# Optimization experiments

Measured on AMD Instinct MI355X. Metric: run time of the kernel, lower is better.

The kernel has to match this reference:

```python
import jax, jax.numpy as jnp
import numpy as np

B, S, D = 16, 4096, 128
LN_EPS = 1e-5
REC_EPS = 1e-8


def setup_inputs() -> dict:
    key = jax.random.key(0)
    k1, k2, k3, k4 = jax.random.split(key, 4)
    return {
        "C": jax.random.normal(k1, (B, S, D), dtype=jnp.float32),
        "V": jax.random.normal(k2, (B, S, D), dtype=jnp.float32),
        "W": jax.random.normal(k3, (B, S, D), dtype=jnp.float32),
        "encoder_context": jax.random.normal(k4, (B, D), dtype=jnp.float32),
        "time_modulation": jnp.full((1, 1, D), 0.5, dtype=jnp.float32),
        "context_modulation": jnp.full((1, D), 0.5, dtype=jnp.float32),
        "ln_weight": jnp.ones((D,), dtype=jnp.float32),
        "ln_bias": jnp.zeros((D,), dtype=jnp.float32),
    }


def reference(C, V, W, encoder_context, time_modulation, context_modulation, ln_weight, ln_bias):
    b_, s_, d_ = C.shape
    tm = time_modulation[0, 0]  # [D]
    # context gate is time-invariant: compute once
    ctx_add = jax.nn.sigmoid(encoder_context * context_modulation) * encoder_context  # [B,D]

    def step(carry, xs):
        a, bst = carry  # a: [B,1], bst: [B,D]
        c_t, v_t, w_t = xs  # each [B,D]
        decay = jax.nn.sigmoid(w_t * tm)  # [B,D]
        ec = jnp.exp(c_t)  # [B,D]
        a = decay.mean(axis=1, keepdims=True) * a + ec.sum(axis=1, keepdims=True)
        bst = decay * bst + ec * v_t + ctx_add
        out_t = bst / (a + REC_EPS)
        return (a, bst), out_t

    a0 = jnp.zeros((b_, 1), dtype=C.dtype)
    b0 = jnp.zeros((b_, d_), dtype=C.dtype)
    xs = (jnp.swapaxes(C, 0, 1), jnp.swapaxes(V, 0, 1), jnp.swapaxes(W, 0, 1))  # [S,B,D]
    _, ys = jax.lax.scan(step, (a0, b0), xs)  # ys: [S,B,D]
    res = jnp.swapaxes(ys, 0, 1)  # [B,S,D]

    mu = jnp.mean(res, axis=-1, keepdims=True)
    var = jnp.var(res, axis=-1, keepdims=True)
    normed = (res - mu) * jax.lax.rsqrt(var + LN_EPS)
    return normed * ln_weight + ln_bias
```

## Files before the change

kernel.cpp:

```cpp
#include <hip/hip_runtime.h>

#define BB   16
#define SS   4096
#define DD   128
#define NCH  512
#define TT   (SS / NCH)
#define WPB  4
#define NTHR 256

#define DTILE 16
#define SUBS  16
#define CPS   (NCH / SUBS)

#define LN_EPS  1e-5f
#define REC_EPS 1e-8f

__device__ __forceinline__ float fast_rcp(float x) { return __builtin_amdgcn_rcpf(x); }
__device__ __forceinline__ float sigm(float x) { return fast_rcp(1.0f + __expf(-x)); }

__device__ __forceinline__ unsigned pack2(float a, float b) {
    unsigned ua = (__float_as_uint(a) + 0x8000u) >> 16;
    unsigned ub = (__float_as_uint(b) + 0x8000u) & 0xFFFF0000u;
    return ub | ua;
}
__device__ __forceinline__ float up_lo(unsigned u) { return __uint_as_float(u << 16); }
__device__ __forceinline__ float up_hi(unsigned u) { return __uint_as_float(u & 0xFFFF0000u); }

template<int CTRL>
__device__ __forceinline__ float dpp_mov0(float x) {
    return __int_as_float(
        __builtin_amdgcn_update_dpp(0, __float_as_int(x), CTRL, 0xF, 0xF, true));
}

__device__ __forceinline__ void wave_red2(float& a, float& b) {
    a += dpp_mov0<0x111>(a); b += dpp_mov0<0x111>(b);
    a += dpp_mov0<0x112>(a); b += dpp_mov0<0x112>(b);
    a += dpp_mov0<0x114>(a); b += dpp_mov0<0x114>(b);
    a += dpp_mov0<0x118>(a); b += dpp_mov0<0x118>(b);
    a += dpp_mov0<0x142>(a); b += dpp_mov0<0x142>(b);
    a += dpp_mov0<0x143>(a); b += dpp_mov0<0x143>(b);
    a = __int_as_float(__builtin_amdgcn_readlane(__float_as_int(a), 63));
    b = __int_as_float(__builtin_amdgcn_readlane(__float_as_int(b), 63));
}

typedef const __attribute__((address_space(1))) unsigned int gas_u32;
typedef __attribute__((address_space(3))) unsigned int las_u32;
__device__ __forceinline__ void gload_lds16(const void* g, void* l) {
    __builtin_amdgcn_global_load_lds((gas_u32*)g, (las_u32*)l, 16, 0, 0);
}

#define VM_WAIT() asm volatile("s_waitcnt vmcnt(0)" ::: "memory")

__global__ __launch_bounds__(NTHR, 3) void pass1_kernel(
    const float* __restrict__ C, const float* __restrict__ V, const float* __restrict__ W,
    const float* __restrict__ enc, const float* __restrict__ tmod, const float* __restrict__ cmod,
    unsigned* __restrict__ DTb,
    float* __restrict__ Pbuf, float* __restrict__ Qbuf,
    float* __restrict__ PaBuf, float* __restrict__ QaBuf,
    float2* __restrict__ MEbuf)
{
    __shared__ float lds[WPB][3][TT * DD];

    const int wv   = threadIdx.x >> 6;
    const int lane = threadIdx.x & 63;
    const int gc   = blockIdx.x * WPB + wv;
    const int b    = gc >> 9;
    const int ch   = gc & (NCH - 1);
    const int d2   = lane << 1;

    const int t0 = ch * TT;
    const size_t chunk = ((size_t)b * SS + t0) * DD;
    const char* Cc = (const char*)(C + chunk);
    const char* Wc = (const char*)(W + chunk);
    const char* Vc = (const char*)(V + chunk);
    uint2* DTp = (uint2*)(DTb + chunk + d2);

#pragma unroll
    for (int i = 0; i < 4; ++i) {
        const size_t bo = (size_t)i * 1024 + (size_t)lane * 16;
        gload_lds16(Cc + bo, &lds[wv][0][i * 256]);
        gload_lds16(Wc + bo, &lds[wv][1][i * 256]);
        gload_lds16(Vc + bo, &lds[wv][2][i * 256]);
    }

    const float2 tm = *(const float2*)(tmod + d2);
    const float2 cm = *(const float2*)(cmod + d2);
    const float2 ec = *(const float2*)(enc + b * DD + d2);

    VM_WAIT();

    float2 ctx;
    ctx.x = sigm(ec.x * cm.x) * ec.x;
    ctx.y = sigm(ec.y * cm.y) * ec.y;

    float2 P = make_float2(1.f, 1.f);
    float2 Q = make_float2(0.f, 0.f);
    float sdp[TT], sep[TT];

#pragma unroll
    for (int t = 0; t < TT; ++t) {
        const float2 cv = *(const float2*)&lds[wv][0][t * DD + d2];
        const float2 wl = *(const float2*)&lds[wv][1][t * DD + d2];
        const float2 vl = *(const float2*)&lds[wv][2][t * DD + d2];

        float2 dec, e2, T2; uint2 u;
        dec.x = sigm(wl.x * tm.x); dec.y = sigm(wl.y * tm.y);
        e2.x = __expf(cv.x); e2.y = __expf(cv.y);
        T2.x = e2.x * vl.x + ctx.x;
        T2.y = e2.y * vl.y + ctx.y;

        u.x = pack2(dec.x, T2.x); u.y = pack2(dec.y, T2.y);
        DTp[t * (DD / 2)] = u;

        const float dqx = up_lo(u.x), dqy = up_lo(u.y);
        const float tqx = up_hi(u.x), tqy = up_hi(u.y);
        Q.x = dqx * Q.x + tqx;
        Q.y = dqy * Q.y + tqy;
        P.x *= dqx; P.y *= dqy;

        sdp[t] = dec.x + dec.y;
        sep[t] = e2.x + e2.y;
    }

#pragma unroll
    for (int t = 0; t < TT; ++t) wave_red2(sdp[t], sep[t]);

    float pa = 1.f, qa = 0.f;
    float mk = 0.f, ek = 0.f;
#pragma unroll
    for (int t = 0; t < TT; ++t) {
        const float mt = sdp[t] * (1.0f / DD);
        pa *= mt;
        qa = mt * qa + sep[t];
        if (lane == t) { mk = mt; ek = sep[t]; }
    }

    *(float2*)(Pbuf + (size_t)gc * DD + d2) = P;
    *(float2*)(Qbuf + (size_t)gc * DD + d2) = Q;
    if (lane < TT) MEbuf[(size_t)b * SS + t0 + lane] = make_float2(mk, ek);
    if (lane == 0) { PaBuf[gc] = pa; QaBuf[gc] = qa; }
}

__global__ __launch_bounds__(256, 2) void pass2_kernel(
    const float* __restrict__ Pbuf, const float* __restrict__ Qbuf,
    const float* __restrict__ PaBuf, const float* __restrict__ QaBuf,
    float* __restrict__ bst0, float* __restrict__ a0)
{
    const int b   = blockIdx.x >> 3;
    const int dt  = blockIdx.x & 7;
    const int tid = threadIdx.x;
    const int dl  = tid & (DTILE - 1);
    const int sub = tid >> 4;
    const int d   = dt * DTILE + dl;

    __shared__ float cP[SUBS][DTILE], cQ[SUBS][DTILE], ent[SUBS][DTILE];
    __shared__ float sPa[256], sQa[256];

    const int ch0 = sub * CPS;
    const size_t base = ((size_t)b * NCH + ch0) * DD + d;
    float Pr[CPS], Qr[CPS];
    float p = 1.f, q = 0.f;
#pragma unroll
    for (int i = 0; i < CPS; ++i) {
        Pr[i] = Pbuf[base + (size_t)i * DD];
        Qr[i] = Qbuf[base + (size_t)i * DD];
        q = Pr[i] * q + Qr[i];
        p = Pr[i] * p;
    }
    cP[sub][dl] = p; cQ[sub][dl] = q;
    __syncthreads();

    if (tid < DTILE) {
        float s = 0.f;
#pragma unroll
        for (int sb = 0; sb < SUBS; ++sb) {
            ent[sb][tid] = s;
            s = cP[sb][tid] * s + cQ[sb][tid];
        }
    }
    __syncthreads();

    float s = ent[sub][dl];
#pragma unroll
    for (int i = 0; i < CPS; ++i) {
        bst0[base + (size_t)i * DD] = s;
        s = Pr[i] * s + Qr[i];
    }

    if (dt == 0) {
        const int cbase = b * NCH;
        const float p0 = PaBuf[cbase + 2 * tid],     q0 = QaBuf[cbase + 2 * tid];
        const float p1 = PaBuf[cbase + 2 * tid + 1], q1 = QaBuf[cbase + 2 * tid + 1];
        float Pc = p1 * p0;
        float Qc = p1 * q0 + q1;
#pragma unroll
        for (int off = 1; off < 256; off <<= 1) {
            sPa[tid] = Pc; sQa[tid] = Qc;
            __syncthreads();
            if (tid >= off) {
                const float pp = sPa[tid - off], qq = sQa[tid - off];
                Qc = Pc * qq + Qc;
                Pc = Pc * pp;
            }
            __syncthreads();
        }
        sQa[tid] = Qc;
        __syncthreads();
        const float E = (tid == 0) ? 0.f : sQa[tid - 1];
        a0[cbase + 2 * tid]     = E;
        a0[cbase + 2 * tid + 1] = p0 * E + q0;
    }
}

__global__ __launch_bounds__(NTHR, 6) void pass3_kernel(
    const unsigned* __restrict__ DTb,
    const float* __restrict__ lnw, const float* __restrict__ lnb,
    const float* __restrict__ bst0, const float* __restrict__ a0,
    const float2* __restrict__ MEbuf,
    float* __restrict__ out)
{
    __shared__ unsigned lds[WPB][TT * DD];

    const int wv   = threadIdx.x >> 6;
    const int lane = threadIdx.x & 63;
    const int gc   = blockIdx.x * WPB + wv;
    const int b    = gc >> 9;
    const int ch   = gc & (NCH - 1);
    const int d2   = lane << 1;

    const int t0 = ch * TT;
    const size_t chunk = ((size_t)b * SS + t0) * DD;
    float2* Op = (float2*)(out + chunk + d2);

    const char* Dc = (const char*)(DTb + chunk);
#pragma unroll
    for (int i = 0; i < 4; ++i)
        gload_lds16(Dc + (size_t)i * 1024 + (size_t)lane * 16, &lds[wv][i * 256]);

    const float2 me = MEbuf[(size_t)b * SS + t0 + (lane & (TT - 1))];
    float2 bst = *(const float2*)(bst0 + (size_t)gc * DD + d2);
    const float a_in = a0[gc];
    const float2 gw = *(const float2*)(lnw + d2);
    const float2 gb = *(const float2*)(lnb + d2);

    VM_WAIT();

    float a = a_in;
    float2 o[TT];
    float s1p[TT], s2p[TT];
#pragma unroll
    for (int t = 0; t < TT; ++t) {
        const float mt = __int_as_float(__builtin_amdgcn_readlane(__float_as_int(me.x), t));
        const float et = __int_as_float(__builtin_amdgcn_readlane(__float_as_int(me.y), t));

        const uint2 dt2 = *(const uint2*)&lds[wv][t * DD + d2];
        a = mt * a + et;
        bst.x = up_lo(dt2.x) * bst.x + up_hi(dt2.x);
        bst.y = up_lo(dt2.y) * bst.y + up_hi(dt2.y);

        const float inva = fast_rcp(a + REC_EPS);
        o[t].x = bst.x * inva; o[t].y = bst.y * inva;
        s1p[t] = o[t].x + o[t].y;
        s2p[t] = o[t].x * o[t].x + o[t].y * o[t].y;
    }

#pragma unroll
    for (int t = 0; t < TT; ++t) wave_red2(s1p[t], s2p[t]);

#pragma unroll
    for (int t = 0; t < TT; ++t) {
        const float mu  = s1p[t] * (1.0f / DD);
        const float var = s2p[t] * (1.0f / DD) - mu * mu;
        const float rs  = rsqrtf(var + LN_EPS);
        float2 r;
        r.x = (o[t].x - mu) * rs * gw.x + gb.x;
        r.y = (o[t].y - mu) * rs * gw.y + gb.y;
        Op[t * (DD / 2)] = r;
    }
}

extern "C" void kernel_launch(void* const* d_in, const int* in_sizes, int n_in,
                              void* d_out, int out_size, void* d_ws, size_t ws_size,
                              hipStream_t stream)
{
    const float* C    = (const float*)d_in[0];
    const float* V    = (const float*)d_in[1];
    const float* W    = (const float*)d_in[2];
    const float* enc  = (const float*)d_in[3];
    const float* tmod = (const float*)d_in[4];
    const float* cmod = (const float*)d_in[5];
    const float* lnw  = (const float*)d_in[6];
    const float* lnb  = (const float*)d_in[7];
    float* out = (float*)d_out;

    float* ws    = (float*)d_ws;
    unsigned* DTbuf = (unsigned*)ws;
    float* Pbuf  = ws    + (size_t)BB * SS * DD;
    float* Qbuf  = Pbuf  + (size_t)BB * NCH * DD;
    float* bst0  = Qbuf  + (size_t)BB * NCH * DD;
    float2* MEbuf = (float2*)(bst0 + (size_t)BB * NCH * DD);
    float* PaBuf = (float*)(MEbuf + (size_t)BB * SS);
    float* QaBuf = PaBuf + (size_t)BB * NCH;
    float* a0Buf = QaBuf + (size_t)BB * NCH;

    const int nblk = BB * NCH / WPB;
    pass1_kernel<<<nblk, NTHR, 0, stream>>>(C, V, W, enc, tmod, cmod, DTbuf,
                                            Pbuf, Qbuf, PaBuf, QaBuf, MEbuf);
    pass2_kernel<<<BB * 8, 256, 0, stream>>>(Pbuf, Qbuf, PaBuf, QaBuf, bst0, a0Buf);
    pass3_kernel<<<nblk, NTHR, 0, stream>>>(DTbuf, lnw, lnb,
                                            bst0, a0Buf, MEbuf, out);
}
```

Baseline: 162.4 us.

## Recompute decay and input terms in pass3 instead of storing packed intermediate buffer

Pass1 no longer writes a bf16-packed decay/input buffer or the per-step mean/exp sums. Pass3 instead reloads C, W and V and recomputes the sigmoid, exp and wave reductions itself. Pass2 is rewritten as one wave per (batch, channel) using a shuffle-based scan, and P/Q are stored interleaved as float2. This removes the intermediate write and read and the bf16 rounding, but costs an extra read of all three inputs and duplicate transcendental work in pass3.

```diff
diff --git a/kernel.cpp b/kernel.cpp
--- a/kernel.cpp
+++ b/kernel.cpp
@@ -7,24 +7,13 @@
 #define TT   (SS / NCH)
 #define WPB  4
 #define NTHR 256
-
-#define DTILE 16
-#define SUBS  16
-#define CPS   (NCH / SUBS)
+#define NWAVE (BB * NCH)
 
 #define LN_EPS  1e-5f
 #define REC_EPS 1e-8f
 
 __device__ __forceinline__ float fast_rcp(float x) { return __builtin_amdgcn_rcpf(x); }
 __device__ __forceinline__ float sigm(float x) { return fast_rcp(1.0f + __expf(-x)); }
-
-__device__ __forceinline__ unsigned pack2(float a, float b) {
-    unsigned ua = (__float_as_uint(a) + 0x8000u) >> 16;
-    unsigned ub = (__float_as_uint(b) + 0x8000u) & 0xFFFF0000u;
-    return ub | ua;
-}
-__device__ __forceinline__ float up_lo(unsigned u) { return __uint_as_float(u << 16); }
-__device__ __forceinline__ float up_hi(unsigned u) { return __uint_as_float(u & 0xFFFF0000u); }
 
 template<int CTRL>
 __device__ __forceinline__ float dpp_mov0(float x) {
@@ -48,16 +37,13 @@
 __device__ __forceinline__ void gload_lds16(const void* g, void* l) {
     __builtin_amdgcn_global_load_lds((gas_u32*)g, (las_u32*)l, 16, 0, 0);
 }
-
 #define VM_WAIT() asm volatile("s_waitcnt vmcnt(0)" ::: "memory")
 
 __global__ __launch_bounds__(NTHR, 3) void pass1_kernel(
     const float* __restrict__ C, const float* __restrict__ V, const float* __restrict__ W,
     const float* __restrict__ enc, const float* __restrict__ tmod, const float* __restrict__ cmod,
-    unsigned* __restrict__ DTb,
-    float* __restrict__ Pbuf, float* __restrict__ Qbuf,
-    float* __restrict__ PaBuf, float* __restrict__ QaBuf,
-    float2* __restrict__ MEbuf)
+    float2* __restrict__ PQ,
+    float2* __restrict__ PaQa)
 {
     __shared__ float lds[WPB][3][TT * DD];
 
@@ -73,7 +59,6 @@
     const char* Cc = (const char*)(C + chunk);
     const char* Wc = (const char*)(W + chunk);
     const char* Vc = (const char*)(V + chunk);
-    uint2* DTp = (uint2*)(DTb + chunk + d2);
 
 #pragma unroll
     for (int i = 0; i < 4; ++i) {
@@ -103,20 +88,15 @@
         const float2 wl = *(const float2*)&lds[wv][1][t * DD + d2];
         const float2 vl = *(const float2*)&lds[wv][2][t * DD + d2];
 
-        float2 dec, e2, T2; uint2 u;
+        float2 dec, e2, T2;
         dec.x = sigm(wl.x * tm.x); dec.y = sigm(wl.y * tm.y);
         e2.x = __expf(cv.x); e2.y = __expf(cv.y);
         T2.x = e2.x * vl.x + ctx.x;
         T2.y = e2.y * vl.y + ctx.y;
 
-        u.x = pack2(dec.x, T2.x); u.y = pack2(dec.y, T2.y);
-        DTp[t * (DD / 2)] = u;
-
-        const float dqx = up_lo(u.x), dqy = up_lo(u.y);
-        const float tqx = up_hi(u.x), tqy = up_hi(u.y);
-        Q.x = dqx * Q.x + tqx;
-        Q.y = dqy * Q.y + tqy;
-        P.x *= dqx; P.y *= dqy;
+        Q.x = dec.x * Q.x + T2.x;
+        Q.y = dec.y * Q.y + T2.y;
+        P.x *= dec.x; P.y *= dec.y;
 
         sdp[t] = dec.x + dec.y;
         sep[t] = e2.x + e2.y;
@@ -126,100 +106,100 @@
     for (int t = 0; t < TT; ++t) wave_red2(sdp[t], sep[t]);
 
     float pa = 1.f, qa = 0.f;
-    float mk = 0.f, ek = 0.f;
 #pragma unroll
     for (int t = 0; t < TT; ++t) {
         const float mt = sdp[t] * (1.0f / DD);
         pa *= mt;
         qa = mt * qa + sep[t];
-        if (lane == t) { mk = mt; ek = sep[t]; }
-    }
-
-    *(float2*)(Pbuf + (size_t)gc * DD + d2) = P;
-    *(float2*)(Qbuf + (size_t)gc * DD + d2) = Q;
-    if (lane < TT) MEbuf[(size_t)b * SS + t0 + lane] = make_float2(mk, ek);
-    if (lane == 0) { PaBuf[gc] = pa; QaBuf[gc] = qa; }
-}
-
-__global__ __launch_bounds__(256, 2) void pass2_kernel(
-    const float* __restrict__ Pbuf, const float* __restrict__ Qbuf,
-    const float* __restrict__ PaBuf, const float* __restrict__ QaBuf,
-    float* __restrict__ bst0, float* __restrict__ a0)
+    }
+
+    float4 pq4;
+    pq4.x = P.x; pq4.y = Q.x; pq4.z = P.y; pq4.w = Q.y;
+    *(float4*)(PQ + (size_t)gc * DD + d2) = pq4;
+    if (lane == 0) PaQa[gc] = make_float2(pa, qa);
+}
+
+__global__ __launch_bounds__(256, 4) void pass2_kernel(
+    const float2* __restrict__ PQ, const float2* __restrict__ PaQa,
+    float* __restrict__ bst0,
+    float* __restrict__ a0)
 {
-    const int b   = blockIdx.x >> 3;
-    const int dt  = blockIdx.x & 7;
-    const int tid = threadIdx.x;
-    const int dl  = tid & (DTILE - 1);
-    const int sub = tid >> 4;
-    const int d   = dt * DTILE + dl;
-
-    __shared__ float cP[SUBS][DTILE], cQ[SUBS][DTILE], ent[SUBS][DTILE];
-    __shared__ float sPa[256], sQa[256];
-
-    const int ch0 = sub * CPS;
-    const size_t base = ((size_t)b * NCH + ch0) * DD + d;
-    float Pr[CPS], Qr[CPS];
-    float p = 1.f, q = 0.f;
-#pragma unroll
-    for (int i = 0; i < CPS; ++i) {
-        Pr[i] = Pbuf[base + (size_t)i * DD];
-        Qr[i] = Qbuf[base + (size_t)i * DD];
-        q = Pr[i] * q + Qr[i];
-        p = Pr[i] * p;
-    }
-    cP[sub][dl] = p; cQ[sub][dl] = q;
-    __syncthreads();
-
-    if (tid < DTILE) {
-        float s = 0.f;
-#pragma unroll
-        for (int sb = 0; sb < SUBS; ++sb) {
-            ent[sb][tid] = s;
-            s = cP[sb][tid] * s + cQ[sb][tid];
+    const int wv   = threadIdx.x >> 6;
+    const int lane = threadIdx.x & 63;
+    const int wid  = blockIdx.x * 4 + wv;
+
+    if (wid < BB * DD) {
+        const int b = wid >> 7;
+        const int d = wid & (DD - 1);
+        const int ch0 = lane * 8;
+        const size_t base = ((size_t)b * NCH + ch0) * DD + d;
+
+        float2 A[8];
+#pragma unroll
+        for (int i = 0; i < 8; ++i) A[i] = PQ[base + (size_t)i * DD];
+
+        float p = 1.f, q = 0.f;
+#pragma unroll
+        for (int i = 0; i < 8; ++i) { q = A[i].x * q + A[i].y; p = A[i].x * p; }
+
+#pragma unroll
+        for (int dl = 1; dl < 64; dl <<= 1) {
+            float ps = __shfl_up(p, dl);
+            float qs = __shfl_up(q, dl);
+            ps = (lane >= dl) ? ps : 1.f;
+            qs = (lane >= dl) ? qs : 0.f;
+            q = p * qs + q;
+            p = p * ps;
         }
-    }
-    __syncthreads();
-
-    float s = ent[sub][dl];
-#pragma unroll
-    for (int i = 0; i < CPS; ++i) {
-        bst0[base + (size_t)i * DD] = s;
-        s = Pr[i] * s + Qr[i];
-    }
-
-    if (dt == 0) {
-        const int cbase = b * NCH;
-        const float p0 = PaBuf[cbase + 2 * tid],     q0 = QaBuf[cbase + 2 * tid];
-        const float p1 = PaBuf[cbase + 2 * tid + 1], q1 = QaBuf[cbase + 2 * tid + 1];
-        float Pc = p1 * p0;
-        float Qc = p1 * q0 + q1;
-#pragma unroll
-        for (int off = 1; off < 256; off <<= 1) {
-            sPa[tid] = Pc; sQa[tid] = Qc;
-            __syncthreads();
-            if (tid >= off) {
-                const float pp = sPa[tid - off], qq = sQa[tid - off];
-                Qc = Pc * qq + Qc;
-                Pc = Pc * pp;
-            }
-            __syncthreads();
+
+        float x = __shfl_up(q, 1);
+        x = (lane >= 1) ? x : 0.f;
+
+#pragma unroll
+        for (int i = 0; i < 8; ++i) {
+            bst0[base + (size_t)i * DD] = x;
+            x = A[i].x * x + A[i].y;
         }
-        sQa[tid] = Qc;
-        __syncthreads();
-        const float E = (tid == 0) ? 0.f : sQa[tid - 1];
-        a0[cbase + 2 * tid]     = E;
-        a0[cbase + 2 * tid + 1] = p0 * E + q0;
-    }
-}
-
-__global__ __launch_bounds__(NTHR, 6) void pass3_kernel(
-    const unsigned* __restrict__ DTb,
+    } else if (wid < BB * DD + BB) {
+        const int b = wid - BB * DD;
+        const int ch0 = lane * 8;
+
+        float2 A[8];
+#pragma unroll
+        for (int i = 0; i < 8; ++i) A[i] = PaQa[b * NCH + ch0 + i];
+
+        float p = 1.f, q = 0.f;
+#pragma unroll
+        for (int i = 0; i < 8; ++i) { q = A[i].x * q + A[i].y; p = A[i].x * p; }
+
+#pragma unroll
+        for (int dl = 1; dl < 64; dl <<= 1) {
+            float ps = __shfl_up(p, dl);
+            float qs = __shfl_up(q, dl);
+            ps = (lane >= dl) ? ps : 1.f;
+            qs = (lane >= dl) ? qs : 0.f;
+            q = p * qs + q;
+            p = p * ps;
+        }
+
+        float x = __shfl_up(q, 1);
+        x = (lane >= 1) ? x : 0.f;
+#pragma unroll
+        for (int i = 0; i < 8; ++i) {
+            a0[b * NCH + ch0 + i] = x;
+            x = A[i].x * x + A[i].y;
+        }
+    }
+}
+
+__global__ __launch_bounds__(NTHR, 3) void pass3_kernel(
+    const float* __restrict__ C, const float* __restrict__ V, const float* __restrict__ W,
+    const float* __restrict__ enc, const float* __restrict__ tmod, const float* __restrict__ cmod,
     const float* __restrict__ lnw, const float* __restrict__ lnb,
     const float* __restrict__ bst0, const float* __restrict__ a0,
-    const float2* __restrict__ MEbuf,
     float* __restrict__ out)
 {
-    __shared__ unsigned lds[WPB][TT * DD];
+    __shared__ float lds[WPB][3][TT * DD];
 
     const int wv   = threadIdx.x >> 6;
     const int lane = threadIdx.x & 63;
@@ -230,33 +210,63 @@
 
     const int t0 = ch * TT;
     const size_t chunk = ((size_t)b * SS + t0) * DD;
+    const char* Cc = (const char*)(C + chunk);
+    const char* Wc = (const char*)(W + chunk);
+    const char* Vc = (const char*)(V + chunk);
     float2* Op = (float2*)(out + chunk + d2);
 
-    const char* Dc = (const char*)(DTb + chunk);
-#pragma unroll
-    for (int i = 0; i < 4; ++i)
-        gload_lds16(Dc + (size_t)i * 1024 + (size_t)lane * 16, &lds[wv][i * 256]);
-
-    const float2 me = MEbuf[(size_t)b * SS + t0 + (lane & (TT - 1))];
+#pragma unroll
+    for (int i = 0; i < 4; ++i) {
+        const size_t bo = (size_t)i * 1024 + (size_t)lane * 16;
+        gload_lds16(Cc + bo, &lds[wv][0][i * 256]);
+        gload_lds16(Wc + bo, &lds[wv][1][i * 256]);
+        gload_lds16(Vc + bo, &lds[wv][2][i * 256]);
+    }
+
+    const float2 tm = *(const float2*)(tmod + d2);
+    const float2 cm = *(const float2*)(cmod + d2);
+    const float2 ec = *(const float2*)(enc + b * DD + d2);
+    const float2 gw = *(const float2*)(lnw + d2);
+    const float2 gb = *(const float2*)(lnb + d2);
     float2 bst = *(const float2*)(bst0 + (size_t)gc * DD + d2);
     const float a_in = a0[gc];
-    const float2 gw = *(const float2*)(lnw + d2);
-    const float2 gb = *(const float2*)(lnb + d2);
 
     VM_WAIT();
+
+    float2 ctx;
+    ctx.x = sigm(ec.x * cm.x) * ec.x;
+    ctx.y = sigm(ec.y * cm.y) * ec.y;
+
+    float sdp[TT], sep[TT];
+#pragma unroll
+    for (int t = 0; t < TT; ++t) {
+        const float2 cv = *(const float2*)&lds[wv][0][t * DD + d2];
+        const float2 wl = *(const float2*)&lds[wv][1][t * DD + d2];
+        sdp[t] = sigm(wl.x * tm.x) + sigm(wl.y * tm.y);
+        sep[t] = __expf(cv.x) + __expf(cv.y);
+    }
+#pragma unroll
+    for (int t = 0; t < TT; ++t) wave_red2(sdp[t], sep[t]);
 
     float a = a_in;
     float2 o[TT];
     float s1p[TT], s2p[TT];
 #pragma unroll
     for (int t = 0; t < TT; ++t) {
-        const float mt = __int_as_float(__builtin_amdgcn_readlane(__float_as_int(me.x), t));
-        const float et = __int_as_float(__builtin_amdgcn_readlane(__float_as_int(me.y), t));
-
-        const uint2 dt2 = *(const uint2*)&lds[wv][t * DD + d2];
-        a = mt * a + et;
-        bst.x = up_lo(dt2.x) * bst.x + up_hi(dt2.x);
-        bst.y = up_lo(dt2.y) * bst.y + up_hi(dt2.y);
+        const float2 cv = *(const float2*)&lds[wv][0][t * DD + d2];
+        const float2 wl = *(const float2*)&lds[wv][1][t * DD + d2];
+        const float2 vl = *(const float2*)&lds[wv][2][t * DD + d2];
+
+        float2 dec, e2, T2;
+        dec.x = sigm(wl.x * tm.x); dec.y = sigm(wl.y * tm.y);
+        e2.x = __expf(cv.x); e2.y = __expf(cv.y);
+        T2.x = e2.x * vl.x + ctx.x;
+        T2.y = e2.y * vl.y + ctx.y;
+
+        const float mt = sdp[t] * (1.0f / DD);
+        a = mt * a + sep[t];
+        bst.x = dec.x * bst.x + T2.x;
+        bst.y = dec.y * bst.y + T2.y;
 
         const float inva = fast_rcp(a + REC_EPS);
         o[t].x = bst.x * inva; o[t].y = bst.y * inva;
@@ -293,20 +303,14 @@
     const float* lnb  = (const float*)d_in[7];
     float* out = (float*)d_out;
 
-    float* ws    = (float*)d_ws;
-    unsigned* DTbuf = (unsigned*)ws;
-    float* Pbuf  = ws    + (size_t)BB * SS * DD;
-    float* Qbuf  = Pbuf  + (size_t)BB * NCH * DD;
-    float* bst0  = Qbuf  + (size_t)BB * NCH * DD;
-    float2* MEbuf = (float2*)(bst0 + (size_t)BB * NCH * DD);
-    float* PaBuf = (float*)(MEbuf + (size_t)BB * SS);
-    float* QaBuf = PaBuf + (size_t)BB * NCH;
-    float* a0Buf = QaBuf + (size_t)BB * NCH;
-
-    const int nblk = BB * NCH / WPB;
-    pass1_kernel<<<nblk, NTHR, 0, stream>>>(C, V, W, enc, tmod, cmod, DTbuf,
-                                            Pbuf, Qbuf, PaBuf, QaBuf, MEbuf);
-    pass2_kernel<<<BB * 8, 256, 0, stream>>>(Pbuf, Qbuf, PaBuf, QaBuf, bst0, a0Buf);
-    pass3_kernel<<<nblk, NTHR, 0, stream>>>(DTbuf, lnw, lnb,
-                                            bst0, a0Buf, MEbuf, out);
-}
+    float2* PQ   = (float2*)d_ws;
+    float2* PaQa = PQ + (size_t)NWAVE * DD;
+    float*  bst0 = (float*)(PaQa + NWAVE);
+    float*  a0   = bst0 + (size_t)NWAVE * DD;
+
+    const int nblk = NWAVE / WPB;
+    pass1_kernel<<<nblk, NTHR, 0, stream>>>(C, V, W, enc, tmod, cmod, PQ, PaQa);
+    pass2_kernel<<<(BB * DD + BB) / 4, 256, 0, stream>>>(PQ, PaQa, bst0, a0);
+    pass3_kernel<<<nblk, NTHR, 0, stream>>>(C, V, W, enc, tmod, cmod, lnw, lnb,
+                                            bst0, a0, out);
+}
```

After: 167.7 us. +3.3%, slower.
